# Kernel optimization log

Measured on AMD Instinct MI355X. Metric: run time of the kernel, lower is better.

The kernel has to match this reference:

```python
import jax, jax.numpy as jnp
import numpy as np
from jax import lax

L1_PENALTY = 0.01
ALPHA = L1_PENALTY / (2.0 * 1024.0)  # matches self.l1_penalty = l1_penalty / (2*1024)
N_ITERS = 200      # fixed FISTA iteration budget (replaces sklearn CD to tol=1e-6)
POWER_ITERS = 30   # power iterations for Lipschitz constant


def setup_inputs() -> dict:
    key = jax.random.key(0)
    k1, k2 = jax.random.split(key)
    D = jax.random.normal(k1, (10000, 1024), dtype=jnp.float32)
    D = D / (jnp.linalg.norm(D, axis=1, keepdims=True) + 1e-12)  # unit-norm concept embeddings
    emb = jax.random.normal(k2, (128, 1024), dtype=jnp.float32)
    emb = emb / (jnp.linalg.norm(emb, axis=1, keepdims=True) + 1e-12)  # unit-norm CLIP embeddings
    return {"embedding": emb, "dictionary": D}


def _lipschitz(D):
    # Largest eigenvalue of (1/n) * X^T X where X = D.T (n = clip_dim = n_samples in sklearn's Lasso objective)
    n = jnp.asarray(D.shape[1], D.dtype)
    v = jnp.ones((D.shape[0],), D.dtype)

    def body(i, v):
        u = v @ D                 # [d]
        v = (u @ D.T) / n         # [K]
        return v / (jnp.linalg.norm(v) + 1e-12)

    v = lax.fori_loop(0, POWER_ITERS, body, v)
    u = v @ D
    return jnp.linalg.norm((u @ D.T) / n)


def _nn_lasso_fista(D, Y):
    # Batched nonnegative Lasso: min_w (1/(2n))||y - D^T w||^2 + alpha*||w||_1, w >= 0
    # Same objective sklearn.linear_model.Lasso(alpha, positive=True, fit_intercept=False) solves per sample.
    n = jnp.asarray(D.shape[1], D.dtype)
    L = _lipschitz(D)
    step = 1.0 / L
    thresh = step * jnp.asarray(ALPHA, D.dtype)
    B, K = Y.shape[0], D.shape[0]
    w0 = jnp.zeros((B, K), Y.dtype)

    def body(i, carry):
        w, z, t = carry
        grad = ((z @ D - Y) @ D.T) / n                 # [B,K] gradient of smooth part
        w_new = jnp.maximum(z - step * grad - thresh, 0.0)  # nonnegative soft-threshold prox
        t_new = 0.5 * (1.0 + jnp.sqrt(1.0 + 4.0 * t * t))
        z_new = w_new + ((t - 1.0) / t_new) * (w_new - w)
        return (w_new, z_new, t_new)

    w, _, _ = lax.fori_loop(0, N_ITERS, body, (w0, w0, jnp.asarray(1.0, Y.dtype)))
    return w


def reference(embedding, dictionary):
    # decompose: per-sample nonnegative Lasso weights, batched
    weights = _nn_lasso_fista(dictionary, embedding)          # [B, K]
    # recompose_vector: weights @ dictionary, then L2-normalize rows
    recon = weights @ dictionary                              # [B, d]
    recon = recon / (jnp.linalg.norm(recon, axis=1, keepdims=True) + 1e-12)
    # encode_vector: diag(recon @ embedding.T).sum() == sum_i <recon_i, emb_i>
    score = jnp.sum(recon * embedding)
    return (weights, score)
```

## Files before the change

kernel.cpp:

```cpp
#include <hip/hip_runtime.h>
#include <math.h>

#define N_ITERS 200
#define PRECISE_TAIL 16
#define FAST_ITERS (N_ITERS - PRECISE_TAIL)
#define B_DIM 128
#define K_DIM 10000
#define KP2 10240
#define KB  10048
#define D_DIM 1024
#define ALPHA_F 4.8828125e-6f
#define SPLITK 32
#define KSLICE 320
#define NSTEP1 10
#define LSCALE 2048.0f
#define INV_LSCALE 4.8828125e-4f

typedef unsigned short u16;
typedef __attribute__((ext_vector_type(8))) _Float16 f16x8;
typedef __attribute__((ext_vector_type(4))) float f32x4;
#define MFMA16 __builtin_amdgcn_mfma_f32_16x16x32_f16

__device__ __forceinline__ u16 f2h(float x) {
    _Float16 h = (_Float16)x;
    return __builtin_bit_cast(unsigned short, h);
}
__device__ __forceinline__ float h2f(u16 v) {
    _Float16 h = __builtin_bit_cast(_Float16, v);
    return (float)h;
}
__device__ __forceinline__ void split2h(float x, u16& h, u16& l) {
    u16 hh = f2h(x);
    h = hh;
    l = f2h((x - h2f(hh)) * LSCALE);
}
__device__ __forceinline__ int swz(int r) { return (r & 3) ^ ((r >> 2) & 1); }

__device__ __forceinline__ void gl2lds16(const u16* g, u16* l) {
    __builtin_amdgcn_global_load_lds(
        (const __attribute__((address_space(1))) unsigned int*)g,
        (__attribute__((address_space(3))) unsigned int*)l,
        16, 0, 0);
}

template<int TN, int KS, bool SP>
__device__ __forceinline__ void gcore(
        const u16* __restrict__ Ahg, const u16* __restrict__ Alg, size_t sA, int arow0,
        const u16* __restrict__ Bhg, const u16* __restrict__ Blg, size_t sB, int brow0,
        size_t k0, int nsteps, u16* lds, int t, f32x4 (*acc)[2]) {
    constexpr int MFRAG = (TN == 64) ? 4 : 2;
    constexpr int P = KS / 32;
    constexpr int NA = P * (SP ? 2 : 1);
    constexpr int AB0 = NA * 4096;
    constexpr int BPAN = TN * 32;
    constexpr int NBP = P * (SP ? 2 : 1);
    constexpr int BUFS = AB0 + NBP * BPAN;
    constexpr int LA = 2 * NA;
    constexpr int LB = (TN == 64) ? (SP ? 2 : 1) : 1;
    constexpr int NLD = LA + LB;
    int lane = t & 63, quad = lane >> 4, lr = lane & 15;
    int wv = t >> 6;
    int wm = (TN == 64) ? ((wv >> 1) * 64) : (wv * 32);
    int wn = (TN == 64) ? ((wv & 1) * 32) : 0;
    int r1 = t >> 2, qs = t & 3;
    int q1 = qs ^ swz(r1);
    const u16* pA[NA][2];
    #pragma unroll
    for (int pa = 0; pa < NA; ++pa) {
        const u16* base = (!SP || pa < P) ? Ahg : Alg;
        size_t kk = k0 + (size_t)(pa % P) * 32;
        pA[pa][0] = base + (size_t)(arow0 + r1) * sA + kk + q1 * 8;
        pA[pa][1] = base + (size_t)(arow0 + r1 + 64) * sA + kk + q1 * 8;
    }
    const u16* pB0;
    const u16* pB1 = nullptr;
    int bdst;
    if constexpr (TN == 64) {
        pB0 = Bhg + (size_t)(brow0 + r1) * sB + k0 + q1 * 8;
        if constexpr (SP) pB1 = Blg + (size_t)(brow0 + r1) * sB + k0 + q1 * 8;
        bdst = AB0 + t * 8;
    } else {
        int j = t >> 7;
        int rb = (t & 127) >> 2;
        int qb = qs ^ swz(rb);
        if constexpr (SP) {
            pB0 = (j ? Blg : Bhg) + (size_t)(brow0 + rb) * sB + k0 + qb * 8;
        } else {
            pB0 = Bhg + (size_t)(brow0 + rb) * sB + k0 + (size_t)j * 32 + qb * 8;
        }
        bdst = AB0 + j * BPAN + (t & 127) * 8;
    }
    int dA = t * 8;
    int offA[MFRAG], offB[2];
    #pragma unroll
    for (int mi = 0; mi < MFRAG; ++mi) { int rr = wm + mi * 16 + lr; offA[mi] = rr * 32 + ((quad ^ swz(rr)) * 8); }
    #pragma unroll
    for (int ni = 0; ni < 2; ++ni) { int rr = wn + ni * 16 + lr; offB[ni] = rr * 32 + ((quad ^ swz(rr)) * 8); }
    f32x4 accC[MFRAG][2];
    #pragma unroll
    for (int mi = 0; mi < MFRAG; ++mi)
        #pragma unroll
        for (int ni = 0; ni < 2; ++ni) { acc[mi][ni] = (f32x4){0.f,0.f,0.f,0.f}; accC[mi][ni] = (f32x4){0.f,0.f,0.f,0.f}; }

    auto stage = [&](u16* b, int c) {
        #pragma unroll
        for (int pa = 0; pa < NA; ++pa) {
            gl2lds16(pA[pa][0] + c, b + pa * 4096 + dA);
            gl2lds16(pA[pa][1] + c, b + pa * 4096 + 2048 + dA);
        }
        gl2lds16(pB0 + c, b + bdst);
        if constexpr (TN == 64 && SP) gl2lds16(pB1 + c, b + bdst + BPAN);
    };
    stage(lds, 0);
    if (nsteps > 1) stage(lds + BUFS, KS);

    for (int s = 0; s < nsteps; ++s) {
        if (s + 2 < nsteps) stage(lds + ((s + 2) % 3) * BUFS, (s + 2) * KS);
        if (s + 3 <= nsteps) {
            asm volatile("s_waitcnt vmcnt(%0)" : : "i"(2 * NLD) : "memory");
        } else if (s + 2 == nsteps) {
            asm volatile("s_waitcnt vmcnt(%0)" : : "i"(NLD) : "memory");
        } else {
            asm volatile("s_waitcnt vmcnt(0)" : : : "memory");
        }
        __builtin_amdgcn_s_barrier();
        u16* b = lds + (s % 3) * BUFS;
        #pragma unroll
        for (int p = 0; p < P; ++p) {
            f16x8 aH[MFRAG], bH[2];
            #pragma unroll
            for (int mi = 0; mi < MFRAG; ++mi) aH[mi] = *(const f16x8*)&b[p * 4096 + offA[mi]];
            #pragma unroll
            for (int ni = 0; ni < 2; ++ni) bH[ni] = *(const f16x8*)&b[AB0 + p * BPAN + offB[ni]];
            if constexpr (SP) {
                f16x8 aL[MFRAG], bL[2];
                #pragma unroll
                for (int mi = 0; mi < MFRAG; ++mi) aL[mi] = *(const f16x8*)&b[(P + p) * 4096 + offA[mi]];
                #pragma unroll
                for (int ni = 0; ni < 2; ++ni) bL[ni] = *(const f16x8*)&b[AB0 + (P + p) * BPAN + offB[ni]];
                #pragma unroll
                for (int mi = 0; mi < MFRAG; ++mi)
                    #pragma unroll
                    for (int ni = 0; ni < 2; ++ni) {
                        acc[mi][ni]  = MFMA16(aH[mi], bH[ni], acc[mi][ni], 0, 0, 0);
                        accC[mi][ni] = MFMA16(aL[mi], bH[ni], accC[mi][ni], 0, 0, 0);
                        accC[mi][ni] = MFMA16(aH[mi], bL[ni], accC[mi][ni], 0, 0, 0);
                    }
            } else {
                #pragma unroll
                for (int mi = 0; mi < MFRAG; ++mi)
                    #pragma unroll
                    for (int ni = 0; ni < 2; ++ni)
                        acc[mi][ni] = MFMA16(aH[mi], bH[ni], acc[mi][ni], 0, 0, 0);
            }
        }
        __builtin_amdgcn_s_barrier();
    }
    if constexpr (SP) {
        #pragma unroll
        for (int mi = 0; mi < MFRAG; ++mi)
            #pragma unroll
            for (int ni = 0; ni < 2; ++ni)
                #pragma unroll
                for (int r = 0; r < 4; ++r)
                    acc[mi][ni][r] += accC[mi][ni][r] * INV_LSCALE;
    }
}

__global__ __launch_bounds__(256) void k_init(float* __restrict__ out,
                                              u16* __restrict__ Zh, u16* __restrict__ Zl,
                                              u16* __restrict__ Wh,
                                              float* __restrict__ u0,
                                              float* __restrict__ scal) {
    int idx = blockIdx.x * 256 + threadIdx.x;
    int stride = gridDim.x * 256;
    for (int i = idx; i <= B_DIM * K_DIM; i += stride) out[i] = 0.0f;
    unsigned* zh = (unsigned*)Zh;
    unsigned* zl = (unsigned*)Zl;
    for (int i = idx; i < B_DIM * KP2 / 2; i += stride) { zh[i] = 0u; zl[i] = 0u; }
    unsigned* wh = (unsigned*)Wh;
    for (int i = idx; i < B_DIM * KB / 2; i += stride) wh[i] = 0u;
    for (int i = idx; i < 64; i += stride) scal[i] = 0.0f;
    for (int i = idx; i < D_DIM; i += stride) u0[i] = 0.0f;
}

__global__ __launch_bounds__(256) void k_convertD(const float* __restrict__ D,
                                                  u16* __restrict__ Dh,
                                                  u16* __restrict__ Dl,
                                                  u16* __restrict__ Dth,
                                                  u16* __restrict__ Dtl) {
    __shared__ u16 Th[32][33], Tl[32][33];
    int tx = threadIdx.x & 31, ty = threadIdx.x >> 5;
    int k0 = blockIdx.x * 32, d0 = blockIdx.y * 32;
    #pragma unroll
    for (int r = 0; r < 4; ++r) {
        int krow = k0 + ty + r * 8;
        float val = (krow < K_DIM) ? D[(size_t)krow * D_DIM + d0 + tx] : 0.0f;
        u16 h, l; split2h(val, h, l);
        if (krow < KB) {
            Dh[(size_t)krow * D_DIM + d0 + tx] = h;
            Dl[(size_t)krow * D_DIM + d0 + tx] = l;
        }
        Th[ty + r * 8][tx] = h;
        Tl[ty + r * 8][tx] = l;
    }
    __syncthreads();
    #pragma unroll
    for (int r = 0; r < 4; ++r) {
        int d = d0 + ty + r * 8;
        int k = k0 + tx;
        Dth[(size_t)d * KP2 + k] = Th[tx][ty + r * 8];
        Dtl[(size_t)d * KP2 + k] = Tl[tx][ty + r * 8];
    }
}

__global__ __launch_bounds__(256) void k_colsum(const float* __restrict__ D,
                                                float* __restrict__ u0) {
    int t = threadIdx.x;
    int kbase = blockIdx.x * 40;
    float a0 = 0.f, a1 = 0.f, a2 = 0.f, a3 = 0.f;
    for (int k = kbase; k < kbase + 40; ++k) {
        const float* row = D + (size_t)k * D_DIM;
        a0 += row[t];
        a1 += row[t + 256];
        a2 += row[t + 512];
        a3 += row[t + 768];
    }
    atomicAdd(&u0[t], a0);
    atomicAdd(&u0[t + 256], a1);
    atomicAdd(&u0[t + 512], a2);
    atomicAdd(&u0[t + 768], a3);
}

__global__ __launch_bounds__(256, 2) void k_gram(const u16* __restrict__ Dth,
                                                 const u16* __restrict__ Dtl,
                                                 float* __restrict__ G) {
    __shared__ __align__(16) u16 lds[3 * 12288];
    int t = threadIdx.x;
    int n0 = blockIdx.x * 64, m0 = blockIdx.y * 128;
    f32x4 acc[4][2];
    gcore<64, 32, true>(Dth, Dtl, KP2, m0, Dth, Dtl, KP2, n0, 0, 320, lds, t, acc);
    int lane = t & 63, quad = lane >> 4, lr = lane & 15;
    int wv = t >> 6;
    int wm = (wv >> 1) * 64, wn = (wv & 1) * 32;
    #pragma unroll
    for (int mi = 0; mi < 4; ++mi)
        #pragma unroll
        for (int ni = 0; ni < 2; ++ni) {
            int c = n0 + wn + ni * 16 + lr;
            #pragma unroll
            for (int r = 0; r < 4; ++r) {
                int row = m0 + wm + mi * 16 + quad * 4 + r;
                G[(size_t)row * D_DIM + c] = acc[mi][ni][r];
            }
        }
}

__global__ __launch_bounds__(256) void k_pstep(const float* __restrict__ G,
                                               const float* __restrict__ u0,
                                               const float* __restrict__ wvin,
                                               float* __restrict__ wvout,
                                               float* __restrict__ scal, int pw) {
    int t = threadIdx.x;
    int c = blockIdx.x * 4 + (t >> 6);
    int lane = t & 63;
    float rsX = (pw > 0) ? rsqrtf(scal[1 + pw]) : 1.0f;
    float a = 0.f;
    const float* Gr = G + (size_t)c * D_DIM;
    #pragma unroll
    for (int j = 0; j < 16; ++j) {
        int r = lane + j * 64;
        float ur = (pw == 0) ? u0[r] : wvin[r] * rsX;
        a = fmaf(ur, Gr[r], a);
    }
    #pragma unroll
    for (int o = 32; o > 0; o >>= 1) a += __shfl_down(a, o, 64);
    if (lane == 0) {
        float uc = (pw == 0) ? u0[c] : wvin[c] * rsX;
        wvout[c] = a;
        atomicAdd(&scal[2 + pw], a * uc);
    }
}

__global__ void k_Lfin(float* __restrict__ scal) {
    float stepv = 1024.0f / sqrtf(scal[2 + 30]);
    scal[0] = stepv;
    scal[1] = stepv * ALPHA_F;
}

__global__ __launch_bounds__(256, 2) void k_g1f(const u16* __restrict__ Zh,
                                                const u16* __restrict__ Dth,
                                                float* __restrict__ Up) {
    __shared__ __align__(16) u16 lds[3 * 6144];
    int t = threadIdx.x;
    int n0 = blockIdx.x * 64;
    int ks = blockIdx.y;
    f32x4 acc[4][2];
    gcore<64, 32, false>(Zh, nullptr, KP2, 0, Dth, nullptr, KP2, n0,
                         (size_t)ks * KSLICE, NSTEP1, lds, t, acc);
    int lane = t & 63, quad = lane >> 4, lr = lane & 15;
    int wv = t >> 6;
    int wm = (wv >> 1) * 64, wn = (wv & 1) * 32;
    float* o = Up + (size_t)ks * (B_DIM * D_DIM);
    #pragma unroll
    for (int mi = 0; mi < 4; ++mi)
        #pragma unroll
        for (int ni = 0; ni < 2; ++ni) {
            int d = n0 + wn + ni * 16 + lr;
            #pragma unroll
            for (int r = 0; r < 4; ++r) {
                int row = wm + mi * 16 + quad * 4 + r;
                o[(size_t)row * D_DIM + d] = acc[mi][ni][r];
            }
        }
}

__global__ __launch_bounds__(256, 2) void k_g1p(const u16* __restrict__ Zh,
                                                const u16* __restrict__ Zl,
                                                const u16* __restrict__ Dth,
                                                const u16* __restrict__ Dtl,
                                                float* __restrict__ Up) {
    __shared__ __align__(16) u16 lds[3 * 12288];
    int t = threadIdx.x;
    int n0 = blockIdx.x * 64;
    int ks = blockIdx.y;
    f32x4 acc[4][2];
    gcore<64, 32, true>(Zh, Zl, KP2, 0, Dth, Dtl, KP2, n0, (size_t)ks * KSLICE,
                        NSTEP1, lds, t, acc);
    int lane = t & 63, quad = lane >> 4, lr = lane & 15;
    int wv = t >> 6;
    int wm = (wv >> 1) * 64, wn = (wv & 1) * 32;
    float* o = Up + (size_t)ks * (B_DIM * D_DIM);
    #pragma unroll
    for (int mi = 0; mi < 4; ++mi)
        #pragma unroll
        for (int ni = 0; ni < 2; ++ni) {
            int d = n0 + wn + ni * 16 + lr;
            #pragma unroll
            for (int r = 0; r < 4; ++r) {
                int row = wm + mi * 16 + quad * 4 + r;
                o[(size_t)row * D_DIM + d] = acc[mi][ni][r];
            }
        }
}

__global__ __launch_bounds__(256) void k_redF(const float* __restrict__ Up,
                                              u16* __restrict__ Eh,
                                              const float* __restrict__ emb) {
    int base = (blockIdx.x * 256 + threadIdx.x) * 8;
    float4 s0 = {0, 0, 0, 0}, s1 = {0, 0, 0, 0};
    #pragma unroll
    for (int s = 0; s < SPLITK; ++s) {
        const float* p = Up + (size_t)s * (B_DIM * D_DIM) + base;
        float4 a = *(const float4*)p;
        float4 b = *(const float4*)(p + 4);
        s0.x += a.x; s0.y += a.y; s0.z += a.z; s0.w += a.w;
        s1.x += b.x; s1.y += b.y; s1.z += b.z; s1.w += b.w;
    }
    float4 e0 = *(const float4*)&emb[base];
    float4 e1 = *(const float4*)&emb[base + 4];
    float vbuf[8] = {s0.x - e0.x, s0.y - e0.y, s0.z - e0.z, s0.w - e0.w,
                     s1.x - e1.x, s1.y - e1.y, s1.z - e1.z, s1.w - e1.w};
    union { u16 us[8]; int4 v; } h;
    #pragma unroll
    for (int q = 0; q < 8; ++q) h.us[q] = f2h(vbuf[q]);
    *(int4*)&Eh[base] = h.v;
}

__global__ __launch_bounds__(256) void k_redP(const float* __restrict__ Up,
                                              u16* __restrict__ Eh,
                                              u16* __restrict__ El,
                                              const float* __restrict__ emb,
                                              int recon) {
    int base = (blockIdx.x * 256 + threadIdx.x) * 8;
    float4 s0 = {0, 0, 0, 0}, s1 = {0, 0, 0, 0};
    #pragma unroll
    for (int s = 0; s < SPLITK; ++s) {
        const float* p = Up + (size_t)s * (B_DIM * D_DIM) + base;
        float4 a = *(const float4*)p;
        float4 b = *(const float4*)(p + 4);
        s0.x += a.x; s0.y += a.y; s0.z += a.z; s0.w += a.w;
        s1.x += b.x; s1.y += b.y; s1.z += b.z; s1.w += b.w;
    }
    if (!recon) {
        float4 e0 = *(const float4*)&emb[base];
        float4 e1 = *(const float4*)&emb[base + 4];
        s0.x -= e0.x; s0.y -= e0.y; s0.z -= e0.z; s0.w -= e0.w;
        s1.x -= e1.x; s1.y -= e1.y; s1.z -= e1.z; s1.w -= e1.w;
    }
    float vbuf[8] = {s0.x, s0.y, s0.z, s0.w, s1.x, s1.y, s1.z, s1.w};
    union { u16 us[8]; int4 v; } h, l;
    #pragma unroll
    for (int q = 0; q < 8; ++q) split2h(vbuf[q], h.us[q], l.us[q]);
    *(int4*)&Eh[base] = h.v;
    *(int4*)&El[base] = l.v;
}

template<int EM>
__global__ __launch_bounds__(256, 2) void k_g2f(const u16* __restrict__ Eh,
                                                const u16* __restrict__ Dh,
                                                u16* __restrict__ Wh,
                                                float* __restrict__ W,
                                                u16* __restrict__ Zh,
                                                u16* __restrict__ Zl,
                                                const float* __restrict__ scal,
                                                float mom) {
    __shared__ __align__(16) u16 lds[3 * 10240];
    int t = threadIdx.x;
    int n0 = blockIdx.x * 32;
    f32x4 acc[2][2];
    gcore<32, 64, false>(Eh, nullptr, D_DIM, 0, Dh, nullptr, D_DIM, n0, 0,
                         16, lds, t, acc);
    int lane = t & 63, quad = lane >> 4, lr = lane & 15;
    int wm = (t >> 6) * 32;
    const float invN = 1.0f / 1024.0f;
    float stepv = scal[0], th = scal[1];
    #pragma unroll
    for (int mi = 0; mi < 2; ++mi)
        #pragma unroll
        for (int ni = 0; ni < 2; ++ni) {
            int k = n0 + ni * 16 + lr;
            #pragma unroll
            for (int r = 0; r < 4; ++r) {
                int i = wm + mi * 16 + quad * 4 + r;
                size_t iz = (size_t)i * KP2 + k;
                float g = acc[mi][ni][r] * invN;
                float z = h2f(Zh[iz]);
                float wold = h2f(Wh[(size_t)i * KB + k]);
                float wnew = fmaxf(z - stepv * g - th, 0.0f);
                float zn = wnew + mom * (wnew - wold);
                if constexpr (EM == 0) {
                    Wh[(size_t)i * KB + k] = f2h(wnew);
                    Zh[iz] = f2h(zn);
                } else {
                    if (k < K_DIM) W[(size_t)i * K_DIM + k] = wnew;
                    u16 h, l; split2h(zn, h, l);
                    Zh[iz] = h; Zl[iz] = l;
                }
            }
        }
}

__global__ __launch_bounds__(256, 2) void k_g2p(const u16* __restrict__ Eh,
                                                const u16* __restrict__ El,
                                                const u16* __restrict__ Dh,
                                                const u16* __restrict__ Dl,
                                                float* __restrict__ W,
                                                u16* __restrict__ Zh, u16* __restrict__ Zl,
                                                const float* __restrict__ scal,
                                                float mom, int writeW) {
    __shared__ __align__(16) u16 lds[3 * 10240];
    int t = threadIdx.x;
    int n0 = blockIdx.x * 32;
    f32x4 acc[2][2];
    gcore<32, 32, true>(Eh, El, D_DIM, 0, Dh, Dl, D_DIM, n0, 0, 32, lds, t, acc);
    int lane = t & 63, quad = lane >> 4, lr = lane & 15;
    int wm = (t >> 6) * 32;
    const float invN = 1.0f / 1024.0f;
    float stepv = scal[0], th = scal[1];
    #pragma unroll
    for (int mi = 0; mi < 2; ++mi)
        #pragma unroll
        for (int ni = 0; ni < 2; ++ni) {
            int k = n0 + ni * 16 + lr;
            #pragma unroll
            for (int r = 0; r < 4; ++r) {
                int i = wm + mi * 16 + quad * 4 + r;
                size_t iz = (size_t)i * KP2 + k;
                float g = acc[mi][ni][r] * invN;
                float z = h2f(Zh[iz]) + h2f(Zl[iz]) * INV_LSCALE;
                float wold = (k < K_DIM) ? W[(size_t)i * K_DIM + k] : 0.0f;
                float wnew = fmaxf(z - stepv * g - th, 0.0f);
                float zn = wnew + mom * (wnew - wold);
                if (k < K_DIM) W[(size_t)i * K_DIM + k] = wnew;
                u16 h, l;
                split2h(writeW ? wnew : zn, h, l);
                Zh[iz] = h; Zl[iz] = l;
            }
        }
}

__global__ __launch_bounds__(256) void k_score(const u16* __restrict__ Eh,
                                               const u16* __restrict__ El,
                                               const float* __restrict__ emb,
                                               float* __restrict__ score) {
    int wid = blockIdx.x * 4 + (threadIdx.x >> 6);
    int lane = threadIdx.x & 63;
    if (wid >= B_DIM) return;
    float rr = 0.f, re = 0.f;
    #pragma unroll
    for (int j = 0; j < D_DIM; j += 64) {
        int idx = wid * D_DIM + j + lane;
        float x = h2f(Eh[idx]) + h2f(El[idx]) * INV_LSCALE;
        rr = fmaf(x, x, rr);
        re = fmaf(x, emb[idx], re);
    }
    #pragma unroll
    for (int off = 32; off > 0; off >>= 1) {
        rr += __shfl_down(rr, off, 64);
        re += __shfl_down(re, off, 64);
    }
    if (lane == 0) atomicAdd(score, re / (sqrtf(rr) + 1e-12f));
}

extern "C" void kernel_launch(void* const* d_in, const int* in_sizes, int n_in,
                              void* d_out, int out_size, void* d_ws, size_t ws_size,
                              hipStream_t stream) {
    const float* emb = (const float*)d_in[0];
    const float* Dm  = (const float*)d_in[1];
    float* out = (float*)d_out;
    float* W = out;

    size_t off = 0;
    auto carve = [&](size_t bytes) -> void* {
        void* r = (char*)d_ws + off;
        off += (bytes + 255) & ~(size_t)255;
        return r;
    };
    float* G    = (float*)carve((size_t)D_DIM * D_DIM * 4);
    float* Up   = (float*)carve((size_t)SPLITK * B_DIM * D_DIM * 4);
    u16*   Zh   = (u16*)carve((size_t)B_DIM * KP2 * 2);
    u16*   Zl   = (u16*)carve((size_t)B_DIM * KP2 * 2);
    u16*   Wh   = (u16*)carve((size_t)B_DIM * KB * 2);
    u16*   Eh   = (u16*)carve((size_t)B_DIM * D_DIM * 2);
    u16*   El   = (u16*)carve((size_t)B_DIM * D_DIM * 2);
    float* u0   = (float*)carve(D_DIM * 4);
    float* wva  = (float*)carve(D_DIM * 4);
    float* wvb  = (float*)carve(D_DIM * 4);
    float* scal = (float*)carve(64 * 4);
    u16*   Dh   = (u16*)carve((size_t)KB * D_DIM * 2);
    u16*   Dl   = (u16*)carve((size_t)KB * D_DIM * 2);
    u16*   Dth  = (u16*)carve((size_t)D_DIM * KP2 * 2);
    u16*   Dtl  = (u16*)carve((size_t)D_DIM * KP2 * 2);

    k_init<<<512, 256, 0, stream>>>(out, Zh, Zl, Wh, u0, scal);
    k_convertD<<<dim3(320, 32), 256, 0, stream>>>(Dm, Dh, Dl, Dth, Dtl);
    k_colsum<<<250, 256, 0, stream>>>(Dm, u0);
    k_gram<<<dim3(16, 8), 256, 0, stream>>>(Dth, Dtl, G);

    for (int pw = 0; pw <= 30; ++pw) {
        float* win  = (pw & 1) ? wva : wvb;
        float* wout = (pw & 1) ? wvb : wva;
        k_pstep<<<256, 256, 0, stream>>>(G, u0, win, wout, scal, pw);
    }
    k_Lfin<<<1, 1, 0, stream>>>(scal);

    double t = 1.0;
    for (int it = 0; it < N_ITERS; ++it) {
        double tn = 0.5 * (1.0 + sqrt(1.0 + 4.0 * t * t));
        float mom = (float)((t - 1.0) / tn);
        t = tn;
        if (it < FAST_ITERS) {
            k_g1f<<<dim3(16, SPLITK), 256, 0, stream>>>(Zh, Dth, Up);
            k_redF<<<64, 256, 0, stream>>>(Up, Eh, emb);
            if (it == FAST_ITERS - 1)
                k_g2f<1><<<dim3(314, 1), 256, 0, stream>>>(Eh, Dh, Wh, W,
                                                           Zh, Zl, scal, mom);
            else
                k_g2f<0><<<dim3(314, 1), 256, 0, stream>>>(Eh, Dh, Wh, W,
                                                           Zh, Zl, scal, mom);
        } else {
            k_g1p<<<dim3(16, SPLITK), 256, 0, stream>>>(Zh, Zl, Dth, Dtl, Up);
            k_redP<<<64, 256, 0, stream>>>(Up, Eh, El, emb, 0);
            k_g2p<<<dim3(314, 1), 256, 0, stream>>>(Eh, El, Dh, Dl, W, Zh, Zl,
                                                    scal, mom,
                                                    (it == N_ITERS - 1) ? 1 : 0);
        }
    }

    k_g1p<<<dim3(16, SPLITK), 256, 0, stream>>>(Zh, Zl, Dth, Dtl, Up);
    k_redP<<<64, 256, 0, stream>>>(Up, Eh, El, emb, 1);
    k_score<<<32, 256, 0, stream>>>(Eh, El, emb, out + (size_t)B_DIM * K_DIM);
}
```

Baseline: 7.893 ms.

## Parameterize LDS pipeline depth, shrink precise tail, widen split-K reduction grid

Makes the number of LDS stage buffers a template parameter and uses five-stage prefetch for the fast Z·D^T split-K GEMM, to hide more global load latency. Reduces the count of final iterations run in split-fp16 precise mode, shifting them to the cheaper single-fp16 path. Rewrites the split-K reduction kernels to one element per thread over many more blocks. Fewer precise iterations risks accuracy of the final weights, and the scalar reductions lose vector loads.

```diff
diff --git a/kernel.cpp b/kernel.cpp
--- a/kernel.cpp
+++ b/kernel.cpp
@@ -2,7 +2,7 @@
 #include <math.h>
 
 #define N_ITERS 200
-#define PRECISE_TAIL 16
+#define PRECISE_TAIL 10
 #define FAST_ITERS (N_ITERS - PRECISE_TAIL)
 #define B_DIM 128
 #define K_DIM 10000
@@ -43,7 +43,7 @@
         16, 0, 0);
 }
 
-template<int TN, int KS, bool SP>
+template<int TN, int KS, bool SP, int NBUF>
 __device__ __forceinline__ void gcore(
         const u16* __restrict__ Ahg, const u16* __restrict__ Alg, size_t sA, int arow0,
         const u16* __restrict__ Bhg, const u16* __restrict__ Blg, size_t sB, int brow0,
@@ -111,20 +111,27 @@
         gl2lds16(pB0 + c, b + bdst);
         if constexpr (TN == 64 && SP) gl2lds16(pB1 + c, b + bdst + BPAN);
     };
-    stage(lds, 0);
-    if (nsteps > 1) stage(lds + BUFS, KS);
+    #pragma unroll
+    for (int i = 0; i < NBUF - 1; ++i)
+        if (i < nsteps) stage(lds + i * BUFS, i * KS);
 
     for (int s = 0; s < nsteps; ++s) {
-        if (s + 2 < nsteps) stage(lds + ((s + 2) % 3) * BUFS, (s + 2) * KS);
-        if (s + 3 <= nsteps) {
+        if (s + NBUF - 1 < nsteps)
+            stage(lds + ((s + NBUF - 1) % NBUF) * BUFS, (s + NBUF - 1) * KS);
+        int rem = nsteps - 1 - s;
+        if (rem >= NBUF - 1) {
+            asm volatile("s_waitcnt vmcnt(%0)" : : "i"((NBUF - 1) * NLD) : "memory");
+        } else if (NBUF >= 5 && rem == 3) {
+            asm volatile("s_waitcnt vmcnt(%0)" : : "i"(3 * NLD) : "memory");
+        } else if (NBUF >= 4 && rem == 2) {
             asm volatile("s_waitcnt vmcnt(%0)" : : "i"(2 * NLD) : "memory");
-        } else if (s + 2 == nsteps) {
+        } else if (rem == 1) {
             asm volatile("s_waitcnt vmcnt(%0)" : : "i"(NLD) : "memory");
         } else {
             asm volatile("s_waitcnt vmcnt(0)" : : : "memory");
         }
         __builtin_amdgcn_s_barrier();
-        u16* b = lds + (s % 3) * BUFS;
+        u16* b = lds + (s % NBUF) * BUFS;
         #pragma unroll
         for (int p = 0; p < P; ++p) {
             f16x8 aH[MFRAG], bH[2];
@@ -239,7 +246,7 @@
     int t = threadIdx.x;
     int n0 = blockIdx.x * 64, m0 = blockIdx.y * 128;
     f32x4 acc[4][2];
-    gcore<64, 32, true>(Dth, Dtl, KP2, m0, Dth, Dtl, KP2, n0, 0, 320, lds, t, acc);
+    gcore<64, 32, true, 3>(Dth, Dtl, KP2, m0, Dth, Dtl, KP2, n0, 0, 320, lds, t, acc);
     int lane = t & 63, quad = lane >> 4, lr = lane & 15;
     int wv = t >> 6;
     int wm = (wv >> 1) * 64, wn = (wv & 1) * 32;
@@ -291,13 +298,13 @@
 __global__ __launch_bounds__(256, 2) void k_g1f(const u16* __restrict__ Zh,
                                                 const u16* __restrict__ Dth,
                                                 float* __restrict__ Up) {
-    __shared__ __align__(16) u16 lds[3 * 6144];
+    __shared__ __align__(16) u16 lds[5 * 6144];
     int t = threadIdx.x;
     int n0 = blockIdx.x * 64;
     int ks = blockIdx.y;
     f32x4 acc[4][2];
-    gcore<64, 32, false>(Zh, nullptr, KP2, 0, Dth, nullptr, KP2, n0,
-                         (size_t)ks * KSLICE, NSTEP1, lds, t, acc);
+    gcore<64, 32, false, 5>(Zh, nullptr, KP2, 0, Dth, nullptr, KP2, n0,
+                            (size_t)ks * KSLICE, NSTEP1, lds, t, acc);
     int lane = t & 63, quad = lane >> 4, lr = lane & 15;
     int wv = t >> 6;
     int wm = (wv >> 1) * 64, wn = (wv & 1) * 32;
@@ -325,8 +332,8 @@
     int n0 = blockIdx.x * 64;
     int ks = blockIdx.y;
     f32x4 acc[4][2];
-    gcore<64, 32, true>(Zh, Zl, KP2, 0, Dth, Dtl, KP2, n0, (size_t)ks * KSLICE,
-                        NSTEP1, lds, t, acc);
+    gcore<64, 32, true, 3>(Zh, Zl, KP2, 0, Dth, Dtl, KP2, n0, (size_t)ks * KSLICE,
+                           NSTEP1, lds, t, acc);
     int lane = t & 63, quad = lane >> 4, lr = lane & 15;
     int wv = t >> 6;
     int wm = (wv >> 1) * 64, wn = (wv & 1) * 32;
@@ -347,24 +354,11 @@
 __global__ __launch_bounds__(256) void k_redF(const float* __restrict__ Up,
                                               u16* __restrict__ Eh,
                                               const float* __restrict__ emb) {
-    int base = (blockIdx.x * 256 + threadIdx.x) * 8;
-    float4 s0 = {0, 0, 0, 0}, s1 = {0, 0, 0, 0};
-    #pragma unroll
-    for (int s = 0; s < SPLITK; ++s) {
-        const float* p = Up + (size_t)s * (B_DIM * D_DIM) + base;
-        float4 a = *(const float4*)p;
-        float4 b = *(const float4*)(p + 4);
-        s0.x += a.x; s0.y += a.y; s0.z += a.z; s0.w += a.w;
-        s1.x += b.x; s1.y += b.y; s1.z += b.z; s1.w += b.w;
-    }
-    float4 e0 = *(const float4*)&emb[base];
-    float4 e1 = *(const float4*)&emb[base + 4];
-    float vbuf[8] = {s0.x - e0.x, s0.y - e0.y, s0.z - e0.z, s0.w - e0.w,
-                     s1.x - e1.x, s1.y - e1.y, s1.z - e1.z, s1.w - e1.w};
-    union { u16 us[8]; int4 v; } h;
-    #pragma unroll
-    for (int q = 0; q < 8; ++q) h.us[q] = f2h(vbuf[q]);
-    *(int4*)&Eh[base] = h.v;
+    int idx = blockIdx.x * 256 + threadIdx.x;
+    float v = 0.f;
+    #pragma unroll
+    for (int s = 0; s < SPLITK; ++s) v += Up[(size_t)s * (B_DIM * D_DIM) + idx];
+    Eh[idx] = f2h(v - emb[idx]);
 }
 
 __global__ __launch_bounds__(256) void k_redP(const float* __restrict__ Up,
@@ -372,28 +366,14 @@
                                               u16* __restrict__ El,
                                               const float* __restrict__ emb,
                                               int recon) {
-    int base = (blockIdx.x * 256 + threadIdx.x) * 8;
-    float4 s0 = {0, 0, 0, 0}, s1 = {0, 0, 0, 0};
-    #pragma unroll
-    for (int s = 0; s < SPLITK; ++s) {
-        const float* p = Up + (size_t)s * (B_DIM * D_DIM) + base;
-        float4 a = *(const float4*)p;
-        float4 b = *(const float4*)(p + 4);
-        s0.x += a.x; s0.y += a.y; s0.z += a.z; s0.w += a.w;
-        s1.x += b.x; s1.y += b.y; s1.z += b.z; s1.w += b.w;
-    }
-    if (!recon) {
-        float4 e0 = *(const float4*)&emb[base];
-        float4 e1 = *(const float4*)&emb[base + 4];
-        s0.x -= e0.x; s0.y -= e0.y; s0.z -= e0.z; s0.w -= e0.w;
-        s1.x -= e1.x; s1.y -= e1.y; s1.z -= e1.z; s1.w -= e1.w;
-    }
-    float vbuf[8] = {s0.x, s0.y, s0.z, s0.w, s1.x, s1.y, s1.z, s1.w};
-    union { u16 us[8]; int4 v; } h, l;
-    #pragma unroll
-    for (int q = 0; q < 8; ++q) split2h(vbuf[q], h.us[q], l.us[q]);
-    *(int4*)&Eh[base] = h.v;
-    *(int4*)&El[base] = l.v;
+    int idx = blockIdx.x * 256 + threadIdx.x;
+    float v = 0.f;
+    #pragma unroll
+    for (int s = 0; s < SPLITK; ++s) v += Up[(size_t)s * (B_DIM * D_DIM) + idx];
+    if (!recon) v -= emb[idx];
+    u16 h, l; split2h(v, h, l);
+    Eh[idx] = h;
+    El[idx] = l;
 }
 
 template<int EM>
@@ -409,8 +389,8 @@
     int t = threadIdx.x;
     int n0 = blockIdx.x * 32;
     f32x4 acc[2][2];
-    gcore<32, 64, false>(Eh, nullptr, D_DIM, 0, Dh, nullptr, D_DIM, n0, 0,
-                         16, lds, t, acc);
+    gcore<32, 64, false, 3>(Eh, nullptr, D_DIM, 0, Dh, nullptr, D_DIM, n0, 0,
+                            16, lds, t, acc);
     int lane = t & 63, quad = lane >> 4, lr = lane & 15;
     int wm = (t >> 6) * 32;
     const float invN = 1.0f / 1024.0f;
@@ -453,7 +433,7 @@
     int t = threadIdx.x;
     int n0 = blockIdx.x * 32;
     f32x4 acc[2][2];
-    gcore<32, 32, true>(Eh, El, D_DIM, 0, Dh, Dl, D_DIM, n0, 0, 32, lds, t, acc);
+    gcore<32, 32, true, 3>(Eh, El, D_DIM, 0, Dh, Dl, D_DIM, n0, 0, 32, lds, t, acc);
     int lane = t & 63, quad = lane >> 4, lr = lane & 15;
     int wm = (t >> 6) * 32;
     const float invN = 1.0f / 1024.0f;
@@ -552,7 +532,7 @@
         t = tn;
         if (it < FAST_ITERS) {
             k_g1f<<<dim3(16, SPLITK), 256, 0, stream>>>(Zh, Dth, Up);
-            k_redF<<<64, 256, 0, stream>>>(Up, Eh, emb);
+            k_redF<<<512, 256, 0, stream>>>(Up, Eh, emb);
             if (it == FAST_ITERS - 1)
                 k_g2f<1><<<dim3(314, 1), 256, 0, stream>>>(Eh, Dh, Wh, W,
                                                            Zh, Zl, scal, mom);
@@ -561,7 +541,7 @@
                                                            Zh, Zl, scal, mom);
         } else {
             k_g1p<<<dim3(16, SPLITK), 256, 0, stream>>>(Zh, Zl, Dth, Dtl, Up);
-            k_redP<<<64, 256, 0, stream>>>(Up, Eh, El, emb, 0);
+            k_redP<<<512, 256, 0, stream>>>(Up, Eh, El, emb, 0);
             k_g2p<<<dim3(314, 1), 256, 0, stream>>>(Eh, El, Dh, Dl, W, Zh, Zl,
                                                     scal, mom,
                                                     (it == N_ITERS - 1) ? 1 : 0);
@@ -569,6 +549,6 @@
     }
 
     k_g1p<<<dim3(16, SPLITK), 256, 0, stream>>>(Zh, Zl, Dth, Dtl, Up);
-    k_redP<<<64, 256, 0, stream>>>(Up, Eh, El, emb, 1);
+    k_redP<<<512, 256, 0, stream>>>(Up, Eh, El, emb, 1);
     k_score<<<32, 256, 0, stream>>>(Eh, El, emb, out + (size_t)B_DIM * K_DIM);
 }
```

Measured after the change: 7.301 ms. 7.5% less time.
